# Optimization experiments

Measured on AMD Instinct MI355X. Metric: run time of the kernel, lower is better.

Reference implementation:

```python
import jax, jax.numpy as jnp
import numpy as np

ANG, CEN = 9, 4
MIND, MAXD = -4, 4
NDISP = MAXD - MIND + 1
BDR = CEN * MAXD  # 16
EPS = 1e-5


def lrelu(x):
    return jnp.where(x >= 0, x, 0.1 * x)


def bn(x, p):
    # p: [4, C] = (gamma, beta, running_mean, running_var); inference-mode BatchNorm
    g, b, m, v = p
    sh = (1, -1) + (1,) * (x.ndim - 2)
    return (x - m.reshape(sh)) * (g.reshape(sh) * jax.lax.rsqrt(v.reshape(sh) + EPS)) + b.reshape(sh)


def conv3d(x, w, pad):
    return jax.lax.conv_general_dilated(
        x, w, (1, 1, 1), [(pad[0], pad[0]), (pad[1], pad[1]), (pad[2], pad[2])],
        dimension_numbers=('NCDHW', 'OIDHW', 'NCDHW'))


def pw3d(x, w, b=None):  # 1x1x1 conv
    y = jnp.einsum('oc,bcdhw->bodhw', w, x)
    return y if b is None else y + b.reshape(1, -1, 1, 1, 1)


def bilinear_zeros(img, px, py):
    # torch F.grid_sample(mode='bilinear', padding_mode='zeros', align_corners=False)
    # img [..., h, w]; px, py: same leading dims + [h, w] (pixel coords)
    h, w = img.shape[-2], img.shape[-1]
    x0 = jnp.floor(px); y0 = jnp.floor(py)
    dx = px - x0; dy = py - y0
    x0i = x0.astype(jnp.int32); y0i = y0.astype(jnp.int32)
    flat = img.reshape(img.shape[:-2] + (h * w,))

    def tap(yi, xi, wgt):
        valid = ((xi >= 0) & (xi < w) & (yi >= 0) & (yi < h)).astype(img.dtype)
        idx = jnp.clip(yi, 0, h - 1) * w + jnp.clip(xi, 0, w - 1)
        v = jnp.take_along_axis(flat, idx.reshape(idx.shape[:-2] + (h * w,)), axis=-1)
        return v.reshape(idx.shape) * wgt * valid

    return (tap(y0i, x0i, (1 - dx) * (1 - dy)) + tap(y0i, x0i + 1, dx * (1 - dy)) +
            tap(y0i + 1, x0i, (1 - dx) * dy) + tap(y0i + 1, x0i + 1, dx * dy))


def generate_mask(lf, disp):
    # lf [b,1,9,9,h,w]; warp() is called with -disp in the torch code
    b, _, _, _, h, w = lf.shape
    imgs = lf[:, 0]                                    # [b,9,9,h,w]
    d = -disp[:, 0]                                    # [b,h,w]
    off = (jnp.arange(ANG) - CEN).astype(imgs.dtype)   # du / dv
    xb = jnp.linspace(0.0, 1.0, w).astype(imgs.dtype)
    yb = jnp.linspace(0.0, 1.0, h).astype(imgs.dtype)
    # grid = 2*(base+shift)-1; align_corners=False pixel coord = ((g+1)*S - 1)/2
    px = (xb[None, None, None, :] + off[None, :, None, None] * d[:, None] / w) * w - 0.5  # [b,9(v),h,w]
    py = (yb[None, None, :, None] + off[None, :, None, None] * d[:, None] / h) * h - 0.5  # [b,9(u),h,w]
    PX = jnp.broadcast_to(px[:, None], (b, ANG, ANG, h, w))
    PY = jnp.broadcast_to(py[:, :, None], (b, ANG, ANG, h, w))
    warped = bilinear_zeros(imgs, PX, PY)
    ref = imgs[:, CEN, CEN][:, None, None]
    diff = jnp.abs(warped - ref)
    diff = diff.at[:, CEN, CEN].set(0.0)  # center view is used unwarped -> zero diff
    return ((1.0 - diff) ** 2).reshape(b, ANG * ANG, h, w)


def build_cost(feat, mask, fuse_w):
    # Direct windowed gather equivalent of the per-disparity Unfold(dilation=h_pad-d)
    # on the angular-tiled padded image. For disparity d and view (ki,kj), output
    # pixel (i,j) reads view (ki,kj) at (i+(CEN-ki)*d, j+(CEN-kj)*d), zeros outside.
    b, c, _, h, w = feat.shape                        # feat [b,8,81,h,w]
    f = feat.reshape(b, c, ANG, ANG, h, w)
    fpad = jnp.pad(f, ((0, 0), (0, 0), (0, 0), (0, 0), (BDR, BDR), (BDR, BDR)))
    ds = jnp.arange(MIND, MAXD + 1)                   # [9]
    ki = jnp.arange(ANG)
    row = BDR + (CEN - ki)[None, :, None] * ds[:, None, None] + jnp.arange(h)[None, None, :]  # [D,9,h]
    col = BDR + (CEN - ki)[None, :, None] * ds[:, None, None] + jnp.arange(w)[None, None, :]  # [D,9,w]
    KI = ki[None, :, None, None, None]
    KJ = ki[None, None, :, None, None]
    RR = row[:, :, None, :, None]
    CC = col[:, None, :, None, :]
    g = fpad[:, :, KI, KJ, RR, CC]                    # [b,8,D,9,9,h,w]
    mod = g * mask.reshape(b, 1, 1, ANG, ANG, h, w)   # mask modulation (ModulateConv2d)
    Wf = fuse_w.reshape(c, fuse_w.shape[0] // c, ANG, ANG)  # grouped 1x1 fuse, groups=c
    cost = jnp.einsum('gouv,bgduvhw->bgodhw', Wf, mod).reshape(b, fuse_w.shape[0], NDISP, h, w)
    return cost / mask.mean(axis=1)[:, None, None]


def _forward(x, dispGT, if_w0, if_bn0, resb_w, resb_b, resb_bn, if_w1, if_bn1,
             if_w2, if_bn2, last_w, fuse_w, sq_w, sq_bn, c1_w, c1_bn, c2_w, c2_bn,
             c3_w, c3_bn, c4_w, r3_body_w, r3_body_bn, r3_ca_w1, r3_ca_b1, r3_ca_bn1,
             r3_ca_w2, r3_ca_b2, r3_ca_bn2):
    b = x.shape[0]
    h = x.shape[2] // ANG; w = x.shape[3] // ANG
    lf = x.reshape(b, 1, ANG, h, ANG, w).transpose(0, 1, 2, 4, 3, 5)  # [b,1,a1,a2,h,w]
    x5 = lf.reshape(b, 1, ANG * ANG, h, w)
    # ---- init_feature: per-view 2D convs expressed as (1,3,3) 3D convs
    hbuf = bn(conv3d(x5, if_w0, (0, 1, 1)), if_bn0)
    for i in range(8):  # 8 ResB blocks (fixed architecture depth)
        t = lrelu(bn(conv3d(hbuf, resb_w[i, 0], (0, 1, 1)) + resb_b[i, 0].reshape(1, -1, 1, 1, 1), resb_bn[i, 0]))
        t = bn(conv3d(t, resb_w[i, 1], (0, 1, 1)) + resb_b[i, 1].reshape(1, -1, 1, 1, 1), resb_bn[i, 1])
        hbuf = hbuf + t
    hbuf = lrelu(bn(conv3d(hbuf, if_w1, (0, 1, 1)), if_bn1))
    hbuf = lrelu(bn(conv3d(hbuf, if_w2, (0, 1, 1)), if_bn2))
    feat = conv3d(hbuf, last_w, (0, 1, 1))            # [b,8,81,h,w]
    # ---- occlusion-aware mask + cost volume
    mask = generate_mask(lf, dispGT)                  # [b,81,h,w]
    cost = build_cost(feat, mask, fuse_w)             # [b,512,9,h,w]
    # ---- 3D CNN aggregation
    buf = lrelu(bn(pw3d(cost, sq_w), sq_bn))
    buf = lrelu(bn(conv3d(buf, c1_w, (1, 1, 1)), c1_bn))
    buf = lrelu(bn(conv3d(buf, c2_w, (1, 1, 1)), c2_bn))
    for i in range(2):  # ResB3D blocks with CALayer
        t = lrelu(bn(conv3d(buf, r3_body_w[i, 0], (1, 1, 1)), r3_body_bn[i, 0]))
        t = bn(conv3d(t, r3_body_w[i, 1], (1, 1, 1)), r3_body_bn[i, 1])
        y = t.mean(axis=(3, 4), keepdims=True)        # AdaptiveAvgPool3d((9,1,1))
        y = lrelu(bn(pw3d(y, r3_ca_w1[i], r3_ca_b1[i]), r3_ca_bn1[i]))
        y = jax.nn.sigmoid(bn(pw3d(y, r3_ca_w2[i], r3_ca_b2[i]), r3_ca_bn2[i]))
        buf = t * y + buf
    buf = lrelu(bn(conv3d(buf, c3_w, (1, 1, 1)), c3_bn))
    score = conv3d(buf, c4_w, (1, 1, 1))[:, 0]        # [b,9,h,w]
    att = jax.nn.softmax(score, axis=1)
    dvals = jnp.arange(MIND, MAXD + 1).astype(att.dtype)
    return jnp.sum(att * dvals[None, :, None, None], axis=1, keepdims=True)  # [b,1,h,w]


def setup_inputs():
    B, H, W = 1, 64, 64
    keys = iter(jax.random.split(jax.random.key(0), 256))

    def nrm(shape, fan_in):
        return jax.random.normal(next(keys), shape, jnp.float32) / np.float32(np.sqrt(fan_in))

    def bnp(c):
        k1, k2, k3, k4 = jax.random.split(next(keys), 4)
        return jnp.stack([jax.random.uniform(k1, (c,), jnp.float32, 0.5, 1.5),
                          0.1 * jax.random.normal(k2, (c,), jnp.float32),
                          0.1 * jax.random.normal(k3, (c,), jnp.float32),
                          jax.random.uniform(k4, (c,), jnp.float32, 0.5, 1.5)])

    d = {}
    d['x'] = jax.random.normal(next(keys), (B, 1, ANG * H, ANG * W), jnp.float32)
    d['dispGT'] = jax.random.uniform(next(keys), (B, 1, H, W), jnp.float32, -4.0, 4.0)
    d['if_w0'] = nrm((16, 1, 1, 3, 3), 9)
    d['if_bn0'] = bnp(16)
    d['resb_w'] = nrm((8, 2, 16, 16, 1, 3, 3), 16 * 9)
    d['resb_b'] = 0.01 * jax.random.normal(next(keys), (8, 2, 16), jnp.float32)
    d['resb_bn'] = jnp.stack([jnp.stack([bnp(16), bnp(16)]) for _ in range(8)])
    d['if_w1'] = nrm((16, 16, 1, 3, 3), 16 * 9)
    d['if_bn1'] = bnp(16)
    d['if_w2'] = nrm((8, 16, 1, 3, 3), 16 * 9)
    d['if_bn2'] = bnp(8)
    d['last_w'] = nrm((8, 8, 1, 3, 3), 8 * 9)
    d['fuse_w'] = nrm((512, 81), 81)
    d['sq_w'] = nrm((160, 512), 512)
    d['sq_bn'] = bnp(160)
    for nmn in ('c1', 'c2', 'c3'):
        d[nmn + '_w'] = nrm((160, 160, 3, 3, 3), 160 * 27)
        d[nmn + '_bn'] = bnp(160)
    d['c4_w'] = nrm((1, 160, 3, 3, 3), 160 * 27)
    d['r3_body_w'] = nrm((2, 2, 160, 160, 3, 3, 3), 160 * 27)
    d['r3_body_bn'] = jnp.stack([jnp.stack([bnp(160), bnp(160)]) for _ in range(2)])
    d['r3_ca_w1'] = nrm((2, 10, 160), 160)
    d['r3_ca_b1'] = 0.01 * jax.random.normal(next(keys), (2, 10), jnp.float32)
    d['r3_ca_bn1'] = jnp.stack([bnp(10) for _ in range(2)])
    d['r3_ca_w2'] = nrm((2, 160, 10), 10)
    d['r3_ca_b2'] = 0.01 * jax.random.normal(next(keys), (2, 160), jnp.float32)
    d['r3_ca_bn2'] = jnp.stack([bnp(160) for _ in range(2)])
    return d


def reference(x, dispGT, if_w0, if_bn0, resb_w, resb_b, resb_bn, if_w1, if_bn1,
              if_w2, if_bn2, last_w, fuse_w, sq_w, sq_bn, c1_w, c1_bn, c2_w, c2_bn,
              c3_w, c3_bn, c4_w, r3_body_w, r3_body_bn, r3_ca_w1, r3_ca_b1, r3_ca_bn1,
              r3_ca_w2, r3_ca_b2, r3_ca_bn2):
    return _forward(x, dispGT, if_w0, if_bn0, resb_w, resb_b, resb_bn, if_w1, if_bn1,
                    if_w2, if_bn2, last_w, fuse_w, sq_w, sq_bn, c1_w, c1_bn, c2_w, c2_bn,
                    c3_w, c3_bn, c4_w, r3_body_w, r3_body_bn, r3_ca_w1, r3_ca_b1, r3_ca_bn1,
                    r3_ca_w2, r3_ca_b2, r3_ca_bn2)
```

## Files before the change

### kernel.cpp

```cpp
#include <hip/hip_runtime.h>
#include <hip/hip_bf16.h>
#include <math.h>

constexpr float EPSB = 1e-5f;

constexpr int SAS = 69696;
constexpr int SRS = 1056;
constexpr size_t SVOL = 81ull * SAS;

constexpr int PZS = 696960;
constexpr int PYS = 10560;
constexpr size_t PVOL = 11ull * 4356 * 160;

constexpr size_t OFF_SA   = 0;
constexpr size_t OFF_SB   = 5645376;
constexpr size_t OFF_MASK = 11290752;
constexpr size_t OFF_INVM = 11622528;
constexpr size_t OFF_SC   = 11626624;
constexpr size_t OFF_YM   = 11663488;
constexpr size_t OFF_Y2   = 11664928;
constexpr size_t OFF_YMP  = 11666368;
constexpr size_t OFF_PA   = 11712448;
constexpr size_t UOFF_PHA = 38758016;
constexpr size_t UOFF_PHB = 46424576;
constexpr size_t UOFF_SHA = 0;
constexpr size_t UOFF_SHB = 11290752;
constexpr size_t UOFF_WH  = 54091136;
constexpr size_t UOFF_WSH = 63767936;
constexpr size_t UOFF_ABH = 63865216;
constexpr size_t UOFF_ABL = 63972736;

typedef short s16x8 __attribute__((ext_vector_type(8)));
typedef float f32x4 __attribute__((ext_vector_type(4)));
typedef _Float16 h16x8 __attribute__((ext_vector_type(8)));
typedef _Float16 h16x4 __attribute__((ext_vector_type(4)));

__device__ __forceinline__ float lrelu_f(float v) { return v >= 0.f ? v : 0.1f * v; }
__device__ __forceinline__ float b2f(unsigned short s) {
  union { float f; unsigned u; } z; z.u = ((unsigned)s) << 16; return z.f;
}
__device__ __forceinline__ unsigned short f2b(float f) {
  __hip_bfloat16 h = __float2bfloat16(f);
  return *(unsigned short*)&h;
}

__global__ __launch_bounds__(256) void k_if0(const float* __restrict__ x,
                                             const float* __restrict__ w0,
                                             const float* __restrict__ bn0,
                                             _Float16* __restrict__ SHA) {
  int a = blockIdx.x;
  int p = blockIdx.y * 256 + threadIdx.x;
  int y = p >> 6, xx = p & 63;
  int ai = a / 9, aj = a % 9;
  float v[3][3];
#pragma unroll
  for (int dy = 0; dy < 3; ++dy) {
    int gy = y + dy - 1;
#pragma unroll
    for (int dx = 0; dx < 3; ++dx) {
      int gx = xx + dx - 1;
      v[dy][dx] = (gy >= 0 && gy < 64 && gx >= 0 && gx < 64)
                      ? x[(ai * 64 + gy) * 576 + aj * 64 + gx] : 0.f;
    }
  }
  h16x8 o0, o1;
#pragma unroll
  for (int c = 0; c < 16; ++c) {
    float acc = 0.f;
#pragma unroll
    for (int t = 0; t < 9; ++t) acc += w0[c * 9 + t] * v[t / 3][t % 3];
    float g = bn0[c], b = bn0[16 + c], m = bn0[32 + c], vv = bn0[48 + c];
    float val = (acc - m) * (g * rsqrtf(vv + EPSB)) + b;
    if (c < 8) o0[c] = (_Float16)val;
    else       o1[c - 8] = (_Float16)val;
  }
  _Float16* dst = SHA + (size_t)a * SAS + (size_t)(y + 1) * SRS + (size_t)(xx + 1) * 16;
  *(h16x8*)&dst[0] = o0;
  *(h16x8*)&dst[8] = o1;
}

__global__ __launch_bounds__(256) void k_wslice(const float* __restrict__ resb_w,
                                                const float* __restrict__ if1_w,
                                                const float* __restrict__ if2_w,
                                                const float* __restrict__ last_w,
                                                _Float16* __restrict__ WSH) {
  int c = blockIdx.x;
  for (int idx = threadIdx.x; idx < 2560; idx += 256) {
    int o = idx / 160, k = idx % 160;
    int t = k >> 4, ci = k & 15;
    float v = 0.f;
    if (t < 9) {
      if (c < 16)       v = resb_w[((size_t)c * 256 + o * 16 + ci) * 9 + t];
      else if (c == 16) v = if1_w[(size_t)(o * 16 + ci) * 9 + t];
      else if (c == 17) v = (o < 8) ? if2_w[(size_t)(o * 16 + ci) * 9 + t] : 0.f;
      else              v = (o < 8 && ci < 8) ? last_w[(size_t)(o * 8 + ci) * 9 + t] : 0.f;
    }
    WSH[c * 2560 + idx] = (_Float16)v;
  }
}

__global__ __launch_bounds__(256) void k_wt7(const float* __restrict__ c1,
                                             const float* __restrict__ c2,
                                             const float* __restrict__ r3,
                                             const float* __restrict__ c3,
                                             _Float16* __restrict__ WH) {
  __shared__ float L[6912];
  int l = blockIdx.y;
  const float* w = (l == 0) ? c1 : (l == 1) ? c2 : (l < 6) ? r3 + (size_t)(l - 2) * 691200 : c3;
  size_t base = (size_t)blockIdx.x * 256;
  for (int i = threadIdx.x; i < 6912; i += 256) L[i] = w[base * 27 + i];
  __syncthreads();
  _Float16* wh = WH + (size_t)l * 691200;
  int r = (int)base + threadIdx.x;
#pragma unroll 1
  for (int t = 0; t < 27; ++t) {
    float v = L[threadIdx.x * 27 + t];
    wh[(size_t)t * 25600 + r] = (_Float16)v;
  }
}

__global__ __launch_bounds__(192) void k_A(const float* __restrict__ sq_w,
                                           const float* __restrict__ fuse_w,
                                           unsigned short* __restrict__ ABH,
                                           unsigned short* __restrict__ ABL) {
  int k = blockIdx.x;
  int o = threadIdx.x;
  if (o >= 160) return;
  float acc = 0.f;
  if (k < 648) {
    int uv = k >> 3, g = k & 7;
    for (int o2 = 0; o2 < 64; ++o2)
      acc += sq_w[(size_t)o * 512 + g * 64 + o2] * fuse_w[(size_t)(g * 64 + o2) * 81 + uv];
  }
  unsigned short h = f2b(acc);
  ABH[(size_t)o * 672 + k] = h;
  ABL[(size_t)o * 672 + k] = f2b(acc - b2f(h));
}

__device__ __forceinline__ float img_at(const float* __restrict__ x, int i, int j, int yy, int xx) {
  if (yy < 0 || yy >= 64 || xx < 0 || xx >= 64) return 0.f;
  return x[(i * 64 + yy) * 576 + j * 64 + xx];
}

__global__ __launch_bounds__(256) void k_mask(const float* __restrict__ x,
                                              const float* __restrict__ disp,
                                              float* __restrict__ mask,
                                              float* __restrict__ invm) {
  int p = blockIdx.x * 256 + threadIdx.x;
  int y = p >> 6, xx = p & 63;
  float d = -disp[p];
  float ref = x[(4 * 64 + y) * 576 + 4 * 64 + xx];
  float ssum = 0.f;
  float xbase = (float)xx * (64.0f / 63.0f);
  float ybase = (float)y * (64.0f / 63.0f);
  for (int i = 0; i < 9; ++i) {
    float py = ybase + (float)(i - 4) * d - 0.5f;
    float y0f = floorf(py);
    float fy = py - y0f;
    int y0 = (int)y0f;
    for (int j = 0; j < 9; ++j) {
      float px = xbase + (float)(j - 4) * d - 0.5f;
      float x0f = floorf(px);
      float fx = px - x0f;
      int x0 = (int)x0f;
      float val = img_at(x, i, j, y0, x0) * (1.f - fx) * (1.f - fy)
                + img_at(x, i, j, y0, x0 + 1) * fx * (1.f - fy)
                + img_at(x, i, j, y0 + 1, x0) * (1.f - fx) * fy
                + img_at(x, i, j, y0 + 1, x0 + 1) * fx * fy;
      float diff = (i == 4 && j == 4) ? 0.f : fabsf(val - ref);
      float m = 1.f - diff;
      m = m * m;
      mask[(i * 9 + j) * 4096 + p] = m;
      ssum += m;
    }
  }
  invm[p] = 81.f / ssum;
}

template <bool BN, bool LRELU, bool RESADD, int CO>
__global__ __launch_bounds__(256) void k_cs(const _Float16* __restrict__ in,
                                            _Float16* __restrict__ out,
                                            const _Float16* __restrict__ wsh,
                                            const float* __restrict__ bias,
                                            const float* __restrict__ bnp) {
  __shared__ _Float16 Af[10 * 66 * 26];
  int a = blockIdx.x, y0 = blockIdx.y * 8;
  int tid = threadIdx.x, lane = tid & 63, w = tid >> 6;
  int lr = lane & 15, lq = lane >> 4;
  const _Float16* src = in + (size_t)a * SAS + (size_t)y0 * SRS;
  for (int it = tid; it < 1320; it += 256) {
    int row = it / 132, rem = it % 132;
    int px = rem >> 1, half = rem & 1;
    h16x8 g = *(const h16x8*)&src[row * SRS + px * 16 + half * 8];
    *(h16x8*)&Af[(row * 66 + px) * 26 + half * 8] = g;
  }
  __syncthreads();
  h16x8 bh[5];
#pragma unroll
  for (int ks = 0; ks < 5; ++ks)
    bh[ks] = *(const h16x8*)&wsh[lr * 160 + ks * 32 + lq * 8];
  int offk[5];
#pragma unroll
  for (int ks = 0; ks < 5; ++ks) {
    int t = ks * 2 + (lq >> 1);
    if (t > 8) t = 8;
    offk[ks] = ((t / 3) * 66 + (t % 3)) * 26 + (lq & 1) * 8;
  }
  f32x4 acc[8];
#pragma unroll
  for (int i = 0; i < 8; ++i) acc[i] = (f32x4){0.f, 0.f, 0.f, 0.f};
#pragma unroll
  for (int mf = 0; mf < 8; ++mf) {
    int gm = w * 8 + mf;
    int yl = gm >> 2, xq = gm & 3;
    int am = (yl * 66 + xq * 16 + lr) * 26;
#pragma unroll
    for (int ks = 0; ks < 5; ++ks) {
      h16x8 ah = *(const h16x8*)&Af[am + offk[ks]];
      acc[mf] = __builtin_amdgcn_mfma_f32_16x16x32_f16(ah, bh[ks], acc[mf], 0, 0, 0);
    }
  }
  int co = lr;
  bool coval = (CO == 16) || (co < CO);
  float sc = 1.f, sh = 0.f;
  if (BN && coval) {
    float g = bnp[co], b = bnp[CO + co], m = bnp[2 * CO + co], vv = bnp[3 * CO + co];
    sc = g * rsqrtf(vv + EPSB);
    sh = b - m * sc;
    if (bias) sh += bias[co] * sc;
  }
#pragma unroll
  for (int mf = 0; mf < 8; ++mf) {
    int gm = w * 8 + mf;
    int yl = gm >> 2, xq = gm & 3;
    if (coval) {
#pragma unroll
      for (int r = 0; r < 4; ++r) {
        int x = xq * 16 + lq * 4 + r;
        float val = acc[mf][r] * sc + sh;
        if (LRELU) val = lrelu_f(val);
        size_t oo = (size_t)a * SAS + (size_t)(y0 + yl + 1) * SRS + (size_t)(x + 1) * 16 + co;
        if (RESADD) out[oo] = (_Float16)((float)out[oo] + val);
        else        out[oo] = (_Float16)val;
      }
    }
  }
}

__global__ __launch_bounds__(256) void k_costsq(const _Float16* __restrict__ feat,
                                                const float* __restrict__ mask,
                                                const float* __restrict__ invm,
                                                const unsigned short* __restrict__ ABH,
                                                const unsigned short* __restrict__ ABL,
                                                const float* __restrict__ sq_bn,
                                                _Float16* __restrict__ outPH) {
  __shared__ short Ah[6144];
  __shared__ short Al[6144];
  int dI = blockIdx.x, y = blockIdx.y;
  int dd = dI - 4;
  int tid = threadIdx.x, lane = tid & 63, w = tid >> 6;
  int wm = w >> 1, wn = w & 1;
  int lr = lane & 15, lq = lane >> 4;
  f32x4 acc[2][5];
#pragma unroll
  for (int i = 0; i < 2; ++i)
#pragma unroll
    for (int j = 0; j < 5; ++j) acc[i][j] = (f32x4){0.f, 0.f, 0.f, 0.f};

  for (int ch = 0; ch < 7; ++ch) {
    __syncthreads();
    for (int it = tid; it < 768; it += 256) {
      int xl = it / 12, uvL = it % 12;
      int uv = ch * 12 + uvL;
      s16x8 hv = {0, 0, 0, 0, 0, 0, 0, 0}, lv = {0, 0, 0, 0, 0, 0, 0, 0};
      if (uv < 81) {
        int u = uv / 9, v = uv % 9;
        int ys = y + (4 - u) * dd;
        int xs = xl + (4 - v) * dd;
        if (ys >= 0 && ys < 64 && xs >= 0 && xs < 64) {
          const _Float16* fp = feat + (size_t)uv * SAS + (size_t)(ys + 1) * SRS + (size_t)(xs + 1) * 16;
          h16x8 fv = *(const h16x8*)fp;
          float mv = mask[uv * 4096 + y * 64 + xl];
#pragma unroll
          for (int j = 0; j < 8; ++j) {
            float f = (float)fv[j] * mv;
            unsigned short h = f2b(f);
            hv[j] = h;
            lv[j] = f2b(f - b2f(h));
          }
        }
      }
      *(s16x8*)&Ah[xl * 96 + uvL * 8] = hv;
      *(s16x8*)&Al[xl * 96 + uvL * 8] = lv;
    }
    __syncthreads();
#pragma unroll
    for (int kb = 0; kb < 3; ++kb) {
      int ka = kb * 32 + lq * 8;
      s16x8 a0h = *(const s16x8*)&Ah[(wm * 32 + lr) * 96 + ka];
      s16x8 a0l = *(const s16x8*)&Al[(wm * 32 + lr) * 96 + ka];
      s16x8 a1h = *(const s16x8*)&Ah[(wm * 32 + 16 + lr) * 96 + ka];
      s16x8 a1l = *(const s16x8*)&Al[(wm * 32 + 16 + lr) * 96 + ka];
      int kg = ch * 96 + ka;
#pragma unroll
      for (int nf = 0; nf < 5; ++nf) {
        int n = wn * 80 + nf * 16 + lr;
        s16x8 bh = *(const s16x8*)&ABH[(size_t)n * 672 + kg];
        s16x8 bl = *(const s16x8*)&ABL[(size_t)n * 672 + kg];
        acc[0][nf] = __builtin_amdgcn_mfma_f32_16x16x32_bf16(a0h, bh, acc[0][nf], 0, 0, 0);
        acc[0][nf] = __builtin_amdgcn_mfma_f32_16x16x32_bf16(a0h, bl, acc[0][nf], 0, 0, 0);
        acc[0][nf] = __builtin_amdgcn_mfma_f32_16x16x32_bf16(a0l, bh, acc[0][nf], 0, 0, 0);
        acc[1][nf] = __builtin_amdgcn_mfma_f32_16x16x32_bf16(a1h, bh, acc[1][nf], 0, 0, 0);
        acc[1][nf] = __builtin_amdgcn_mfma_f32_16x16x32_bf16(a1h, bl, acc[1][nf], 0, 0, 0);
        acc[1][nf] = __builtin_amdgcn_mfma_f32_16x16x32_bf16(a1l, bh, acc[1][nf], 0, 0, 0);
      }
    }
  }
#pragma unroll
  for (int nf = 0; nf < 5; ++nf) {
    int n = wn * 80 + nf * 16 + lr;
    float g = sq_bn[n], b = sq_bn[160 + n], m = sq_bn[320 + n], vv = sq_bn[480 + n];
    float sc = g * rsqrtf(vv + EPSB), sh = b - m * sc;
#pragma unroll
    for (int mf = 0; mf < 2; ++mf) {
#pragma unroll
      for (int r = 0; r < 4; ++r) {
        int x = wm * 32 + mf * 16 + lq * 4 + r;
        float val = acc[mf][nf][r] * invm[y * 64 + x];
        val = val * sc + sh;
        val = lrelu_f(val);
        outPH[(size_t)(dI + 1) * PZS + (size_t)(y + 1) * PYS + (size_t)(x + 1) * 160 + n] =
            (_Float16)val;
      }
    }
  }
}

template <bool LRELU>
__global__ __launch_bounds__(320, 3) void k_mconv(const _Float16* __restrict__ in,
                                                  float* __restrict__ out32,
                                                  _Float16* __restrict__ out16,
                                                  const _Float16* __restrict__ wh,
                                                  const float* __restrict__ bnp) {
  __shared__ _Float16 Af[66 * 174];
  int bid = blockIdx.x;
  int swz = (bid & 7) * 72 + (bid >> 3);
  int z = swz / 64, y = swz % 64;
  int tid = threadIdx.x;
  int lane = tid & 63;
  int wn = tid >> 6;
  int lr = lane & 15;
  int lq = lane >> 4;

  f32x4 acc[4][2];
#pragma unroll
  for (int i = 0; i < 4; ++i)
#pragma unroll
    for (int j = 0; j < 2; ++j) acc[i][j] = (f32x4){0.f, 0.f, 0.f, 0.f};

  const _Float16* wbase = wh + (size_t)(wn * 32 + lr) * 160 + lq * 8;

#pragma unroll 1
  for (int dzy = 0; dzy < 9; ++dzy) {
    int dz = dzy / 3, dy = dzy % 3;
    const _Float16* src = in + (size_t)(z + dz) * PZS + (size_t)(y + dy) * PYS;
    __syncthreads();
    for (int v = tid; v < 1320; v += 320) {
      h16x8 g = *(const h16x8*)&src[(size_t)v * 8];
      int row = v / 20, col = (v % 20) * 8;
      *(h16x8*)&Af[row * 174 + col] = g;
    }
    __syncthreads();

#pragma unroll 1
    for (int dx = 0; dx < 3; ++dx) {
      const _Float16* wt = wbase + (size_t)(dzy * 3 + dx) * 25600;
      h16x8 bA[2], bB[2];
#pragma unroll
      for (int nf = 0; nf < 2; ++nf)
        bA[nf] = *(const h16x8*)&wt[(size_t)nf * 16 * 160];

      auto step = [&](int ks, h16x8 (&cur)[2], h16x8 (&nxt)[2], bool pre) {
        if (pre) {
#pragma unroll
          for (int nf = 0; nf < 2; ++nf)
            nxt[nf] = *(const h16x8*)&wt[(size_t)nf * 16 * 160 + (ks + 1) * 32];
        }
        h16x8 a0 = *(const h16x8*)&Af[(0 * 16 + lr + dx) * 174 + ks * 32 + lq * 8];
        h16x8 a1 = *(const h16x8*)&Af[(1 * 16 + lr + dx) * 174 + ks * 32 + lq * 8];
        h16x8 a2 = *(const h16x8*)&Af[(2 * 16 + lr + dx) * 174 + ks * 32 + lq * 8];
        h16x8 a3 = *(const h16x8*)&Af[(3 * 16 + lr + dx) * 174 + ks * 32 + lq * 8];
#pragma unroll
        for (int nf = 0; nf < 2; ++nf) {
          acc[0][nf] = __builtin_amdgcn_mfma_f32_16x16x32_f16(a0, cur[nf], acc[0][nf], 0, 0, 0);
          acc[1][nf] = __builtin_amdgcn_mfma_f32_16x16x32_f16(a1, cur[nf], acc[1][nf], 0, 0, 0);
          acc[2][nf] = __builtin_amdgcn_mfma_f32_16x16x32_f16(a2, cur[nf], acc[2][nf], 0, 0, 0);
          acc[3][nf] = __builtin_amdgcn_mfma_f32_16x16x32_f16(a3, cur[nf], acc[3][nf], 0, 0, 0);
        }
      };
      step(0, bA, bB, true);
      step(1, bB, bA, true);
      step(2, bA, bB, true);
      step(3, bB, bA, true);
      step(4, bA, bB, false);
    }
  }
#pragma unroll
  for (int nf = 0; nf < 2; ++nf) {
    int n = wn * 32 + nf * 16 + lr;
    float sc = bnp[n] * rsqrtf(bnp[480 + n] + EPSB);
    float sh = bnp[160 + n] - bnp[320 + n] * sc;
#pragma unroll
    for (int mq = 0; mq < 4; ++mq) {
#pragma unroll
      for (int r = 0; r < 4; ++r) {
        int x = mq * 16 + lq * 4 + r;
        float val = acc[mq][nf][r] * sc + sh;
        if (LRELU) val = lrelu_f(val);
        size_t oo = (size_t)(z + 1) * PZS + (size_t)(y + 1) * PYS + (size_t)(x + 1) * 160 + n;
        if (out32) out32[oo] = val;
        if (out16) out16[oo] = (_Float16)val;
      }
    }
  }
}

__global__ __launch_bounds__(256) void k_c4(const _Float16* __restrict__ in,
                                            const float* __restrict__ w,
                                            float* __restrict__ score) {
  __shared__ float L[66 * 169];
  __shared__ float red[256];
  int zy = blockIdx.x;
  int z = zy / 64, y = zy % 64;
  int tid = threadIdx.x;
  int x = tid & 63, q = tid >> 6;
  float acc = 0.f;
  for (int dzy = 0; dzy < 9; ++dzy) {
    int dz = dzy / 3, dy = dzy % 3;
    const _Float16* src = in + (size_t)(z + dz) * PZS + (size_t)(y + dy) * PYS;
    __syncthreads();
    for (int v = tid; v < 1320; v += 256) {
      h16x8 g = *(const h16x8*)&src[v * 8];
      int row = v / 20, col = (v % 20) * 8;
#pragma unroll
      for (int j = 0; j < 8; ++j) L[row * 169 + col + j] = (float)g[j];
    }
    __syncthreads();
#pragma unroll 1
    for (int dx = 0; dx < 3; ++dx) {
      int t = dzy * 3 + dx;
      for (int ci = q * 40; ci < q * 40 + 40; ++ci)
        acc += L[(x + dx) * 169 + ci] * w[ci * 27 + t];
    }
  }
  red[tid] = acc;
  __syncthreads();
  if (q == 0)
    score[z * 4096 + y * 64 + x] = red[x] + red[64 + x] + red[128 + x] + red[192 + x];
}

__global__ __launch_bounds__(256) void k_mean1(const float* __restrict__ in,
                                               float* __restrict__ ymp) {
  int z = blockIdx.x, yg = blockIdx.y, xq = blockIdx.z;
  int c = threadIdx.x;
  if (c >= 160) return;
  float s = 0.f;
  for (int yy = 0; yy < 8; ++yy) {
    int y = yg * 8 + yy;
    for (int xl = 0; xl < 16; ++xl) {
      int x = xq * 16 + xl;
      s += in[(size_t)(z + 1) * PZS + (size_t)(y + 1) * PYS + (size_t)(x + 1) * 160 + c];
    }
  }
  ymp[((z * 8 + yg) * 4 + xq) * 160 + c] = s;
}

__global__ __launch_bounds__(256) void k_mean2(const float* __restrict__ ymp,
                                               float* __restrict__ ym) {
  int idx = blockIdx.x * 256 + threadIdx.x;
  if (idx >= 1440) return;
  int c = idx / 9, z = idx % 9;
  float s = 0.f;
  for (int p = 0; p < 32; ++p) s += ymp[(z * 32 + p) * 160 + c];
  ym[idx] = s * (1.f / 4096.f);
}

__global__ __launch_bounds__(256) void k_ca(const float* __restrict__ ym,
                                            const float* __restrict__ w1,
                                            const float* __restrict__ b1,
                                            const float* __restrict__ bn1,
                                            const float* __restrict__ w2,
                                            const float* __restrict__ b2,
                                            const float* __restrict__ bn2,
                                            float* __restrict__ y2) {
  __shared__ float yml[1440];
  __shared__ float yy[90];
  for (int i = threadIdx.x; i < 1440; i += 256) yml[i] = ym[i];
  __syncthreads();
  if (threadIdx.x < 90) {
    int c = threadIdx.x / 9, z = threadIdx.x % 9;
    float acc = b1[c];
    for (int ci = 0; ci < 160; ++ci) acc += w1[c * 160 + ci] * yml[ci * 9 + z];
    float g = bn1[c], b = bn1[10 + c], m = bn1[20 + c], vv = bn1[30 + c];
    acc = (acc - m) * (g * rsqrtf(vv + EPSB)) + b;
    yy[threadIdx.x] = lrelu_f(acc);
  }
  __syncthreads();
  for (int i = threadIdx.x; i < 1440; i += 256) {
    int c = i / 9, z = i % 9;
    float acc = b2[c];
#pragma unroll
    for (int k = 0; k < 10; ++k) acc += w2[c * 10 + k] * yy[k * 9 + z];
    float g = bn2[c], b = bn2[160 + c], m = bn2[320 + c], vv = bn2[480 + c];
    acc = (acc - m) * (g * rsqrtf(vv + EPSB)) + b;
    y2[i] = 1.f / (1.f + expf(-acc));
  }
}

__global__ __launch_bounds__(256) void k_sadd(float* __restrict__ buf,
                                              _Float16* __restrict__ shadow,
                                              const float* __restrict__ t,
                                              const float* __restrict__ y2) {
  int i = blockIdx.x * 256 + threadIdx.x;
  int p = i / 160, c = i % 160;
  int z = p >> 12, r = p & 4095;
  int y = r >> 6, x = r & 63;
  size_t a = (size_t)(z + 1) * PZS + (size_t)(y + 1) * PYS + (size_t)(x + 1) * 160 + c;
  float val = buf[a] + t[a] * y2[c * 9 + z];
  buf[a] = val;
  shadow[a] = (_Float16)val;
}

__global__ __launch_bounds__(256) void k_out(const float* __restrict__ score,
                                             float* __restrict__ out) {
  int p = blockIdx.x * 256 + threadIdx.x;
  float v[9];
  float mx = -1e30f;
#pragma unroll
  for (int z = 0; z < 9; ++z) {
    v[z] = score[z * 4096 + p];
    mx = fmaxf(mx, v[z]);
  }
  float s = 0.f, r = 0.f;
#pragma unroll
  for (int z = 0; z < 9; ++z) {
    float e = expf(v[z] - mx);
    s += e;
    r += e * (float)(z - 4);
  }
  out[p] = r / s;
}

extern "C" void kernel_launch(void* const* d_in, const int* in_sizes, int n_in,
                              void* d_out, int out_size, void* d_ws, size_t ws_size,
                              hipStream_t stream) {
  const float* X      = (const float*)d_in[0];
  const float* disp   = (const float*)d_in[1];
  const float* if_w0  = (const float*)d_in[2];
  const float* if_bn0 = (const float*)d_in[3];
  const float* resb_w = (const float*)d_in[4];
  const float* resb_b = (const float*)d_in[5];
  const float* resb_bn= (const float*)d_in[6];
  const float* if_w1  = (const float*)d_in[7];
  const float* if_bn1 = (const float*)d_in[8];
  const float* if_w2  = (const float*)d_in[9];
  const float* if_bn2 = (const float*)d_in[10];
  const float* last_w = (const float*)d_in[11];
  const float* fuse_w = (const float*)d_in[12];
  const float* sq_w   = (const float*)d_in[13];
  const float* sq_bn  = (const float*)d_in[14];
  const float* c1_w   = (const float*)d_in[15];
  const float* c1_bn  = (const float*)d_in[16];
  const float* c2_w   = (const float*)d_in[17];
  const float* c2_bn  = (const float*)d_in[18];
  const float* c3_w   = (const float*)d_in[19];
  const float* c3_bn  = (const float*)d_in[20];
  const float* c4_w   = (const float*)d_in[21];
  const float* r3_w   = (const float*)d_in[22];
  const float* r3_bn  = (const float*)d_in[23];
  const float* ca_w1  = (const float*)d_in[24];
  const float* ca_b1  = (const float*)d_in[25];
  const float* ca_bn1 = (const float*)d_in[26];
  const float* ca_w2  = (const float*)d_in[27];
  const float* ca_b2  = (const float*)d_in[28];
  const float* ca_bn2 = (const float*)d_in[29];

  float* ws   = (float*)d_ws;
  float* PC   = ws;
  float* MASK = ws + OFF_MASK;
  float* INVM = ws + OFF_INVM;
  float* SC   = ws + OFF_SC;
  float* YM   = ws + OFF_YM;
  float* Y2   = ws + OFF_Y2;
  float* YMP  = ws + OFF_YMP;
  float* PA   = ws + OFF_PA;
  unsigned short* U   = (unsigned short*)d_ws;
  _Float16* SHA       = (_Float16*)(U + UOFF_SHA);
  _Float16* SHB       = (_Float16*)(U + UOFF_SHB);
  _Float16* PHA       = (_Float16*)(U + UOFF_PHA);
  _Float16* PHB       = (_Float16*)(U + UOFF_PHB);
  _Float16* WH        = (_Float16*)(U + UOFF_WH);
  _Float16* WSS       = (_Float16*)(U + UOFF_WSH);
  unsigned short* ABH = U + UOFF_ABH;
  unsigned short* ABL = U + UOFF_ABL;

  hipMemsetAsync(SHA, 0, SVOL * 2, stream);
  hipMemsetAsync(SHB, 0, SVOL * 2, stream);
  hipMemsetAsync(PHA, 0, PVOL * 2, stream);
  hipMemsetAsync(PHB, 0, PVOL * 2, stream);

  k_wt7<<<dim3(100, 7), 256, 0, stream>>>(c1_w, c2_w, r3_w, c3_w, WH);
  k_wslice<<<19, 256, 0, stream>>>(resb_w, if_w1, if_w2, last_w, WSS);
  k_A<<<672, 192, 0, stream>>>(sq_w, fuse_w, ABH, ABL);
  k_mask<<<16, 256, 0, stream>>>(X, disp, MASK, INVM);

  k_if0<<<dim3(81, 16), 256, 0, stream>>>(X, if_w0, if_bn0, SHA);
  for (int i = 0; i < 8; ++i) {
    k_cs<true, true, false, 16><<<dim3(81, 8), 256, 0, stream>>>(
        SHA, SHB, WSS + (size_t)(2 * i) * 2560, resb_b + i * 32, resb_bn + i * 128);
    k_cs<true, false, true, 16><<<dim3(81, 8), 256, 0, stream>>>(
        SHB, SHA, WSS + (size_t)(2 * i + 1) * 2560, resb_b + i * 32 + 16, resb_bn + i * 128 + 64);
  }
  k_cs<true, true, false, 16><<<dim3(81, 8), 256, 0, stream>>>(
      SHA, SHB, WSS + 16 * 2560, nullptr, if_bn1);
  k_cs<true, true, false, 8><<<dim3(81, 8), 256, 0, stream>>>(
      SHB, SHA, WSS + 17 * 2560, nullptr, if_bn2);
  k_cs<false, false, false, 8><<<dim3(81, 8), 256, 0, stream>>>(
      SHA, SHB, WSS + 18 * 2560, nullptr, nullptr);

  k_costsq<<<dim3(9, 64), 256, 0, stream>>>(SHB, MASK, INVM, ABH, ABL, sq_bn, PHA);

  k_mconv<true><<<576, 320, 0, stream>>>(PHA, nullptr, PHB, WH + 0ull * 691200, c1_bn);
  k_mconv<true><<<576, 320, 0, stream>>>(PHB, PA, PHA, WH + 1ull * 691200, c2_bn);
  for (int i = 0; i < 2; ++i) {
    k_mconv<true><<<576, 320, 0, stream>>>(PHA, nullptr, PHB,
                                           WH + (size_t)(2 + 2 * i) * 691200, r3_bn + i * 1280);
    k_mconv<false><<<576, 320, 0, stream>>>(PHB, PC, nullptr,
                                            WH + (size_t)(3 + 2 * i) * 691200,
                                            r3_bn + i * 1280 + 640);
    k_mean1<<<dim3(9, 8, 4), 256, 0, stream>>>(PC, YMP);
    k_mean2<<<6, 256, 0, stream>>>(YMP, YM);
    k_ca<<<1, 256, 0, stream>>>(YM, ca_w1 + i * 1600, ca_b1 + i * 10, ca_bn1 + i * 40,
                                ca_w2 + i * 1600, ca_b2 + i * 160, ca_bn2 + i * 640, Y2);
    k_sadd<<<23040, 256, 0, stream>>>(PA, PHA, PC, Y2);
  }
  k_mconv<true><<<576, 320, 0, stream>>>(PHA, nullptr, PHB, WH + 6ull * 691200, c3_bn);
  k_c4<<<576, 256, 0, stream>>>(PHB, c4_w, SC);
  k_out<<<16, 256, 0, stream>>>(SC, (float*)d_out);
}
```

Baseline: 980.8 us.

## Fuse residual-block convs, drop split-bf16 cost GEMM, shrink LDS padding

Replaces the two per-residual-block spatial conv launches with one fused kernel that keeps the intermediate activation and residual in LDS. This removes half the launches and the global round-trip of the intermediate. The cost-volume squeeze GEMM now uses a single fp16 MFMA instead of three bf16 hi/lo MFMAs. The r3 conv output is stored as fp16 instead of fp32, and LDS row strides change from 26/174 to 24/168. The fp16 changes cost accuracy, and the new strides may add LDS bank conflicts.

```diff
diff --git a/kernel.cpp b/kernel.cpp
--- a/kernel.cpp
+++ b/kernel.cpp
@@ -12,8 +12,6 @@
 constexpr int PYS = 10560;
 constexpr size_t PVOL = 11ull * 4356 * 160;
 
-constexpr size_t OFF_SA   = 0;
-constexpr size_t OFF_SB   = 5645376;
 constexpr size_t OFF_MASK = 11290752;
 constexpr size_t OFF_INVM = 11622528;
 constexpr size_t OFF_SC   = 11626624;
@@ -21,28 +19,20 @@
 constexpr size_t OFF_Y2   = 11664928;
 constexpr size_t OFF_YMP  = 11666368;
 constexpr size_t OFF_PA   = 11712448;
+constexpr size_t UOFF_SHA = 0;
+constexpr size_t UOFF_SHB = 11290752;
+constexpr size_t UOFF_PHC = 0;
 constexpr size_t UOFF_PHA = 38758016;
 constexpr size_t UOFF_PHB = 46424576;
-constexpr size_t UOFF_SHA = 0;
-constexpr size_t UOFF_SHB = 11290752;
 constexpr size_t UOFF_WH  = 54091136;
 constexpr size_t UOFF_WSH = 63767936;
-constexpr size_t UOFF_ABH = 63865216;
-constexpr size_t UOFF_ABL = 63972736;
-
-typedef short s16x8 __attribute__((ext_vector_type(8)));
+constexpr size_t UOFF_ABF = 63865216;
+
 typedef float f32x4 __attribute__((ext_vector_type(4)));
 typedef _Float16 h16x8 __attribute__((ext_vector_type(8)));
 typedef _Float16 h16x4 __attribute__((ext_vector_type(4)));
 
 __device__ __forceinline__ float lrelu_f(float v) { return v >= 0.f ? v : 0.1f * v; }
-__device__ __forceinline__ float b2f(unsigned short s) {
-  union { float f; unsigned u; } z; z.u = ((unsigned)s) << 16; return z.f;
-}
-__device__ __forceinline__ unsigned short f2b(float f) {
-  __hip_bfloat16 h = __float2bfloat16(f);
-  return *(unsigned short*)&h;
-}
 
 __global__ __launch_bounds__(256) void k_if0(const float* __restrict__ x,
                                              const float* __restrict__ w0,
@@ -121,8 +111,7 @@
 
 __global__ __launch_bounds__(192) void k_A(const float* __restrict__ sq_w,
                                            const float* __restrict__ fuse_w,
-                                           unsigned short* __restrict__ ABH,
-                                           unsigned short* __restrict__ ABL) {
+                                           _Float16* __restrict__ ABF) {
   int k = blockIdx.x;
   int o = threadIdx.x;
   if (o >= 160) return;
@@ -132,9 +121,7 @@
     for (int o2 = 0; o2 < 64; ++o2)
       acc += sq_w[(size_t)o * 512 + g * 64 + o2] * fuse_w[(size_t)(g * 64 + o2) * 81 + uv];
   }
-  unsigned short h = f2b(acc);
-  ABH[(size_t)o * 672 + k] = h;
-  ABL[(size_t)o * 672 + k] = f2b(acc - b2f(h));
+  ABF[(size_t)o * 672 + k] = (_Float16)acc;
 }
 
 __device__ __forceinline__ float img_at(const float* __restrict__ x, int i, int j, int yy, int xx) {
@@ -177,13 +164,12 @@
   invm[p] = 81.f / ssum;
 }
 
-template <bool BN, bool LRELU, bool RESADD, int CO>
+template <bool BN, bool LRELU, int CO>
 __global__ __launch_bounds__(256) void k_cs(const _Float16* __restrict__ in,
                                             _Float16* __restrict__ out,
                                             const _Float16* __restrict__ wsh,
-                                            const float* __restrict__ bias,
                                             const float* __restrict__ bnp) {
-  __shared__ _Float16 Af[10 * 66 * 26];
+  __shared__ _Float16 Af[15840];
   int a = blockIdx.x, y0 = blockIdx.y * 8;
   int tid = threadIdx.x, lane = tid & 63, w = tid >> 6;
   int lr = lane & 15, lq = lane >> 4;
@@ -192,7 +178,7 @@
     int row = it / 132, rem = it % 132;
     int px = rem >> 1, half = rem & 1;
     h16x8 g = *(const h16x8*)&src[row * SRS + px * 16 + half * 8];
-    *(h16x8*)&Af[(row * 66 + px) * 26 + half * 8] = g;
+    *(h16x8*)&Af[(row * 66 + px) * 24 + half * 8] = g;
   }
   __syncthreads();
   h16x8 bh[5];
@@ -204,7 +190,7 @@
   for (int ks = 0; ks < 5; ++ks) {
     int t = ks * 2 + (lq >> 1);
     if (t > 8) t = 8;
-    offk[ks] = ((t / 3) * 66 + (t % 3)) * 26 + (lq & 1) * 8;
+    offk[ks] = ((t / 3) * 66 + (t % 3)) * 24 + (lq & 1) * 8;
   }
   f32x4 acc[8];
 #pragma unroll
@@ -213,7 +199,7 @@
   for (int mf = 0; mf < 8; ++mf) {
     int gm = w * 8 + mf;
     int yl = gm >> 2, xq = gm & 3;
-    int am = (yl * 66 + xq * 16 + lr) * 26;
+    int am = (yl * 66 + xq * 16 + lr) * 24;
 #pragma unroll
     for (int ks = 0; ks < 5; ++ks) {
       h16x8 ah = *(const h16x8*)&Af[am + offk[ks]];
@@ -227,7 +213,6 @@
     float g = bnp[co], b = bnp[CO + co], m = bnp[2 * CO + co], vv = bnp[3 * CO + co];
     sc = g * rsqrtf(vv + EPSB);
     sh = b - m * sc;
-    if (bias) sh += bias[co] * sc;
   }
 #pragma unroll
   for (int mf = 0; mf < 8; ++mf) {
@@ -240,8 +225,99 @@
         float val = acc[mf][r] * sc + sh;
         if (LRELU) val = lrelu_f(val);
         size_t oo = (size_t)a * SAS + (size_t)(y0 + yl + 1) * SRS + (size_t)(x + 1) * 16 + co;
-        if (RESADD) out[oo] = (_Float16)((float)out[oo] + val);
-        else        out[oo] = (_Float16)val;
+        out[oo] = (_Float16)val;
+      }
+    }
+  }
+}
+
+__global__ __launch_bounds__(256, 2) void k_cs2(const _Float16* __restrict__ in,
+                                                _Float16* __restrict__ out,
+                                                const _Float16* __restrict__ w1,
+                                                const _Float16* __restrict__ w2,
+                                                const float* __restrict__ bias,
+                                                const float* __restrict__ bnp) {
+  __shared__ _Float16 L1[12 * 66 * 24];
+  __shared__ _Float16 L2[10 * 66 * 24];
+  int a = blockIdx.x, y0 = blockIdx.y * 8;
+  int tid = threadIdx.x, lane = tid & 63, w = tid >> 6;
+  int lr = lane & 15, lq = lane >> 4;
+  for (int i = tid; i < 1980; i += 256) ((h16x8*)L2)[i] = (h16x8)(_Float16)0.f;
+  const _Float16* src = in + (size_t)a * SAS;
+  for (int it = tid; it < 1584; it += 256) {
+    int sr = it / 132, rem = it % 132;
+    int px = rem >> 1, half = rem & 1;
+    int gyp = y0 - 1 + sr;
+    h16x8 g = (h16x8)(_Float16)0.f;
+    if (gyp >= 0 && gyp <= 65)
+      g = *(const h16x8*)&src[(size_t)gyp * SRS + px * 16 + half * 8];
+    *(h16x8*)&L1[(sr * 66 + px) * 24 + half * 8] = g;
+  }
+  __syncthreads();
+  int offk[5];
+#pragma unroll
+  for (int ks = 0; ks < 5; ++ks) {
+    int t = ks * 2 + (lq >> 1);
+    if (t > 8) t = 8;
+    offk[ks] = ((t / 3) * 66 + (t % 3)) * 24 + (lq & 1) * 8;
+  }
+  {
+    h16x8 bh[5];
+#pragma unroll
+    for (int ks = 0; ks < 5; ++ks)
+      bh[ks] = *(const h16x8*)&w1[lr * 160 + ks * 32 + lq * 8];
+    float g1 = bnp[lr], b1 = bnp[16 + lr], m1 = bnp[32 + lr], v1 = bnp[48 + lr];
+    float sc1 = g1 * rsqrtf(v1 + EPSB);
+    float sh1 = b1 - m1 * sc1 + bias[lr] * sc1;
+#pragma unroll
+    for (int mf = 0; mf < 10; ++mf) {
+      int gm = w * 10 + mf;
+      int yl = gm >> 2, xq = gm & 3;
+      f32x4 acc = (f32x4){0.f, 0.f, 0.f, 0.f};
+      int am = (yl * 66 + xq * 16 + lr) * 24;
+#pragma unroll
+      for (int ks = 0; ks < 5; ++ks) {
+        h16x8 ah = *(const h16x8*)&L1[am + offk[ks]];
+        acc = __builtin_amdgcn_mfma_f32_16x16x32_f16(ah, bh[ks], acc, 0, 0, 0);
+      }
+      int gy = y0 - 1 + yl;
+      if (gy >= 0 && gy <= 63) {
+#pragma unroll
+        for (int r = 0; r < 4; ++r) {
+          int x = xq * 16 + lq * 4 + r;
+          float val = lrelu_f(acc[r] * sc1 + sh1);
+          L2[(yl * 66 + x + 1) * 24 + lr] = (_Float16)val;
+        }
+      }
+    }
+  }
+  __syncthreads();
+  {
+    h16x8 bh[5];
+#pragma unroll
+    for (int ks = 0; ks < 5; ++ks)
+      bh[ks] = *(const h16x8*)&w2[lr * 160 + ks * 32 + lq * 8];
+    float g2 = bnp[64 + lr], b2 = bnp[80 + lr], m2 = bnp[96 + lr], v2 = bnp[112 + lr];
+    float sc2 = g2 * rsqrtf(v2 + EPSB);
+    float sh2 = b2 - m2 * sc2 + bias[16 + lr] * sc2;
+#pragma unroll
+    for (int mf = 0; mf < 8; ++mf) {
+      int gm = w * 8 + mf;
+      int yl = gm >> 2, xq = gm & 3;
+      f32x4 acc = (f32x4){0.f, 0.f, 0.f, 0.f};
+      int am = (yl * 66 + xq * 16 + lr) * 24;
+#pragma unroll
+      for (int ks = 0; ks < 5; ++ks) {
+        h16x8 ah = *(const h16x8*)&L2[am + offk[ks]];
+        acc = __builtin_amdgcn_mfma_f32_16x16x32_f16(ah, bh[ks], acc, 0, 0, 0);
+      }
+#pragma unroll
+      for (int r = 0; r < 4; ++r) {
+        int x = xq * 16 + lq * 4 + r;
+        float res = (float)L1[((yl + 2) * 66 + x + 1) * 24 + lr];
+        float val = res + acc[r] * sc2 + sh2;
+        out[(size_t)a * SAS + (size_t)(y0 + yl + 1) * SRS + (size_t)(x + 1) * 16 + lr] =
+            (_Float16)val;
       }
     }
   }
@@ -250,12 +326,10 @@
 __global__ __launch_bounds__(256) void k_costsq(const _Float16* __restrict__ feat,
                                                 const float* __restrict__ mask,
                                                 const float* __restrict__ invm,
-                                                const unsigned short* __restrict__ ABH,
-                                                const unsigned short* __restrict__ ABL,
+                                                const _Float16* __restrict__ ABF,
                                                 const float* __restrict__ sq_bn,
                                                 _Float16* __restrict__ outPH) {
-  __shared__ short Ah[6144];
-  __shared__ short Al[6144];
+  __shared__ _Float16 Ahs[6144];
   int dI = blockIdx.x, y = blockIdx.y;
   int dd = dI - 4;
   int tid = threadIdx.x, lane = tid & 63, w = tid >> 6;
@@ -272,7 +346,7 @@
     for (int it = tid; it < 768; it += 256) {
       int xl = it / 12, uvL = it % 12;
       int uv = ch * 12 + uvL;
-      s16x8 hv = {0, 0, 0, 0, 0, 0, 0, 0}, lv = {0, 0, 0, 0, 0, 0, 0, 0};
+      h16x8 hv = (h16x8)(_Float16)0.f;
       if (uv < 81) {
         int u = uv / 9, v = uv % 9;
         int ys = y + (4 - u) * dd;
@@ -282,37 +356,24 @@
           h16x8 fv = *(const h16x8*)fp;
           float mv = mask[uv * 4096 + y * 64 + xl];
 #pragma unroll
-          for (int j = 0; j < 8; ++j) {
-            float f = (float)fv[j] * mv;
-            unsigned short h = f2b(f);
-            hv[j] = h;
-            lv[j] = f2b(f - b2f(h));
-          }
+          for (int j = 0; j < 8; ++j) hv[j] = (_Float16)((float)fv[j] * mv);
         }
       }
-      *(s16x8*)&Ah[xl * 96 + uvL * 8] = hv;
-      *(s16x8*)&Al[xl * 96 + uvL * 8] = lv;
+      *(h16x8*)&Ahs[xl * 96 + uvL * 8] = hv;
     }
     __syncthreads();
 #pragma unroll
     for (int kb = 0; kb < 3; ++kb) {
       int ka = kb * 32 + lq * 8;
-      s16x8 a0h = *(const s16x8*)&Ah[(wm * 32 + lr) * 96 + ka];
-      s16x8 a0l = *(const s16x8*)&Al[(wm * 32 + lr) * 96 + ka];
-      s16x8 a1h = *(const s16x8*)&Ah[(wm * 32 + 16 + lr) * 96 + ka];
-      s16x8 a1l = *(const s16x8*)&Al[(wm * 32 + 16 + lr) * 96 + ka];
+      h16x8 a0 = *(const h16x8*)&Ahs[(wm * 32 + lr) * 96 + ka];
+      h16x8 a1 = *(const h16x8*)&Ahs[(wm * 32 + 16 + lr) * 96 + ka];
       int kg = ch * 96 + ka;
 #pragma unroll
       for (int nf = 0; nf < 5; ++nf) {
         int n = wn * 80 + nf * 16 + lr;
-        s16x8 bh = *(const s16x8*)&ABH[(size_t)n * 672 + kg];
-        s16x8 bl = *(const s16x8*)&ABL[(size_t)n * 672 + kg];
-        acc[0][nf] = __builtin_amdgcn_mfma_f32_16x16x32_bf16(a0h, bh, acc[0][nf], 0, 0, 0);
-        acc[0][nf] = __builtin_amdgcn_mfma_f32_16x16x32_bf16(a0h, bl, acc[0][nf], 0, 0, 0);
-        acc[0][nf] = __builtin_amdgcn_mfma_f32_16x16x32_bf16(a0l, bh, acc[0][nf], 0, 0, 0);
-        acc[1][nf] = __builtin_amdgcn_mfma_f32_16x16x32_bf16(a1h, bh, acc[1][nf], 0, 0, 0);
-        acc[1][nf] = __builtin_amdgcn_mfma_f32_16x16x32_bf16(a1h, bl, acc[1][nf], 0, 0, 0);
-        acc[1][nf] = __builtin_amdgcn_mfma_f32_16x16x32_bf16(a1l, bh, acc[1][nf], 0, 0, 0);
+        h16x8 bf = *(const h16x8*)&ABF[(size_t)n * 672 + kg];
+        acc[0][nf] = __builtin_amdgcn_mfma_f32_16x16x32_f16(a0, bf, acc[0][nf], 0, 0, 0);
+        acc[1][nf] = __builtin_amdgcn_mfma_f32_16x16x32_f16(a1, bf, acc[1][nf], 0, 0, 0);
       }
     }
   }
@@ -342,7 +403,7 @@
                                                   _Float16* __restrict__ out16,
                                                   const _Float16* __restrict__ wh,
                                                   const float* __restrict__ bnp) {
-  __shared__ _Float16 Af[66 * 174];
+  __shared__ _Float16 Af[66 * 168];
   int bid = blockIdx.x;
   int swz = (bid & 7) * 72 + (bid >> 3);
   int z = swz / 64, y = swz % 64;
@@ -368,7 +429,7 @@
     for (int v = tid; v < 1320; v += 320) {
       h16x8 g = *(const h16x8*)&src[(size_t)v * 8];
       int row = v / 20, col = (v % 20) * 8;
-      *(h16x8*)&Af[row * 174 + col] = g;
+      *(h16x8*)&Af[row * 168 + col] = g;
     }
     __syncthreads();
 
@@ -386,10 +447,10 @@
           for (int nf = 0; nf < 2; ++nf)
             nxt[nf] = *(const h16x8*)&wt[(size_t)nf * 16 * 160 + (ks + 1) * 32];
         }
-        h16x8 a0 = *(const h16x8*)&Af[(0 * 16 + lr + dx) * 174 + ks * 32 + lq * 8];
-        h16x8 a1 = *(const h16x8*)&Af[(1 * 16 + lr + dx) * 174 + ks * 32 + lq * 8];
-        h16x8 a2 = *(const h16x8*)&Af[(2 * 16 + lr + dx) * 174 + ks * 32 + lq * 8];
-        h16x8 a3 = *(const h16x8*)&Af[(3 * 16 + lr + dx) * 174 + ks * 32 + lq * 8];
+        h16x8 a0 = *(const h16x8*)&Af[(0 * 16 + lr + dx) * 168 + ks * 32 + lq * 8];
+        h16x8 a1 = *(const h16x8*)&Af[(1 * 16 + lr + dx) * 168 + ks * 32 + lq * 8];
+        h16x8 a2 = *(const h16x8*)&Af[(2 * 16 + lr + dx) * 168 + ks * 32 + lq * 8];
+        h16x8 a3 = *(const h16x8*)&Af[(3 * 16 + lr + dx) * 168 + ks * 32 + lq * 8];
 #pragma unroll
         for (int nf = 0; nf < 2; ++nf) {
           acc[0][nf] = __builtin_amdgcn_mfma_f32_16x16x32_f16(a0, cur[nf], acc[0][nf], 0, 0, 0);
@@ -459,7 +520,7 @@
     score[z * 4096 + y * 64 + x] = red[x] + red[64 + x] + red[128 + x] + red[192 + x];
 }
 
-__global__ __launch_bounds__(256) void k_mean1(const float* __restrict__ in,
+__global__ __launch_bounds__(256) void k_mean1(const _Float16* __restrict__ in,
                                                float* __restrict__ ymp) {
   int z = blockIdx.x, yg = blockIdx.y, xq = blockIdx.z;
   int c = threadIdx.x;
@@ -469,7 +530,7 @@
     int y = yg * 8 + yy;
     for (int xl = 0; xl < 16; ++xl) {
       int x = xq * 16 + xl;
-      s += in[(size_t)(z + 1) * PZS + (size_t)(y + 1) * PYS + (size_t)(x + 1) * 160 + c];
+      s += (float)in[(size_t)(z + 1) * PZS + (size_t)(y + 1) * PYS + (size_t)(x + 1) * 160 + c];
     }
   }
   ymp[((z * 8 + yg) * 4 + xq) * 160 + c] = s;
@@ -519,14 +580,14 @@
 
 __global__ __launch_bounds__(256) void k_sadd(float* __restrict__ buf,
                                               _Float16* __restrict__ shadow,
-                                              const float* __restrict__ t,
+                                              const _Float16* __restrict__ t,
                                               const float* __restrict__ y2) {
   int i = blockIdx.x * 256 + threadIdx.x;
   int p = i / 160, c = i % 160;
   int z = p >> 12, r = p & 4095;
   int y = r >> 6, x = r & 63;
   size_t a = (size_t)(z + 1) * PZS + (size_t)(y + 1) * PYS + (size_t)(x + 1) * 160 + c;
-  float val = buf[a] + t[a] * y2[c * 9 + z];
+  float val = buf[a] + (float)t[a] * y2[c * 9 + z];
   buf[a] = val;
   shadow[a] = (_Float16)val;
 }
@@ -586,7 +647,6 @@
   const float* ca_bn2 = (const float*)d_in[29];
 
   float* ws   = (float*)d_ws;
-  float* PC   = ws;
   float* MASK = ws + OFF_MASK;
   float* INVM = ws + OFF_INVM;
   float* SC   = ws + OFF_SC;
@@ -597,12 +657,12 @@
   unsigned short* U   = (unsigned short*)d_ws;
   _Float16* SHA       = (_Float16*)(U + UOFF_SHA);
   _Float16* SHB       = (_Float16*)(U + UOFF_SHB);
+  _Float16* PHC       = (_Float16*)(U + UOFF_PHC);
   _Float16* PHA       = (_Float16*)(U + UOFF_PHA);
   _Float16* PHB       = (_Float16*)(U + UOFF_PHB);
   _Float16* WH        = (_Float16*)(U + UOFF_WH);
   _Float16* WSS       = (_Float16*)(U + UOFF_WSH);
-  unsigned short* ABH = U + UOFF_ABH;
-  unsigned short* ABL = U + UOFF_ABL;
+  _Float16* ABF       = (_Float16*)(U + UOFF_ABF);
 
   hipMemsetAsync(SHA, 0, SVOL * 2, stream);
   hipMemsetAsync(SHB, 0, SVOL * 2, stream);
@@ -611,38 +671,36 @@
 
   k_wt7<<<dim3(100, 7), 256, 0, stream>>>(c1_w, c2_w, r3_w, c3_w, WH);
   k_wslice<<<19, 256, 0, stream>>>(resb_w, if_w1, if_w2, last_w, WSS);
-  k_A<<<672, 192, 0, stream>>>(sq_w, fuse_w, ABH, ABL);
+  k_A<<<672, 192, 0, stream>>>(sq_w, fuse_w, ABF);
   k_mask<<<16, 256, 0, stream>>>(X, disp, MASK, INVM);
 
   k_if0<<<dim3(81, 16), 256, 0, stream>>>(X, if_w0, if_bn0, SHA);
   for (int i = 0; i < 8; ++i) {
-    k_cs<true, true, false, 16><<<dim3(81, 8), 256, 0, stream>>>(
-        SHA, SHB, WSS + (size_t)(2 * i) * 2560, resb_b + i * 32, resb_bn + i * 128);
-    k_cs<true, false, true, 16><<<dim3(81, 8), 256, 0, stream>>>(
-        SHB, SHA, WSS + (size_t)(2 * i + 1) * 2560, resb_b + i * 32 + 16, resb_bn + i * 128 + 64);
-  }
-  k_cs<true, true, false, 16><<<dim3(81, 8), 256, 0, stream>>>(
-      SHA, SHB, WSS + 16 * 2560, nullptr, if_bn1);
-  k_cs<true, true, false, 8><<<dim3(81, 8), 256, 0, stream>>>(
-      SHB, SHA, WSS + 17 * 2560, nullptr, if_bn2);
-  k_cs<false, false, false, 8><<<dim3(81, 8), 256, 0, stream>>>(
-      SHA, SHB, WSS + 18 * 2560, nullptr, nullptr);
-
-  k_costsq<<<dim3(9, 64), 256, 0, stream>>>(SHB, MASK, INVM, ABH, ABL, sq_bn, PHA);
+    _Float16* src = (i & 1) ? SHB : SHA;
+    _Float16* dst = (i & 1) ? SHA : SHB;
+    k_cs2<<<dim3(81, 8), 256, 0, stream>>>(
+        src, dst, WSS + (size_t)(2 * i) * 2560, WSS + (size_t)(2 * i + 1) * 2560,
+        resb_b + i * 32, resb_bn + i * 128);
+  }
+  k_cs<true, true, 16><<<dim3(81, 8), 256, 0, stream>>>(SHA, SHB, WSS + 16 * 2560, if_bn1);
+  k_cs<true, true, 8><<<dim3(81, 8), 256, 0, stream>>>(SHB, SHA, WSS + 17 * 2560, if_bn2);
+  k_cs<false, false, 8><<<dim3(81, 8), 256, 0, stream>>>(SHA, SHB, WSS + 18 * 2560, nullptr);
+
+  k_costsq<<<dim3(9, 64), 256, 0, stream>>>(SHB, MASK, INVM, ABF, sq_bn, PHA);
 
   k_mconv<true><<<576, 320, 0, stream>>>(PHA, nullptr, PHB, WH + 0ull * 691200, c1_bn);
   k_mconv<true><<<576, 320, 0, stream>>>(PHB, PA, PHA, WH + 1ull * 691200, c2_bn);
   for (int i = 0; i < 2; ++i) {
     k_mconv<true><<<576, 320, 0, stream>>>(PHA, nullptr, PHB,
                                            WH + (size_t)(2 + 2 * i) * 691200, r3_bn + i * 1280);
-    k_mconv<false><<<576, 320, 0, stream>>>(PHB, PC, nullptr,
+    k_mconv<false><<<576, 320, 0, stream>>>(PHB, nullptr, PHC,
                                             WH + (size_t)(3 + 2 * i) * 691200,
                                             r3_bn + i * 1280 + 640);
-    k_mean1<<<dim3(9, 8, 4), 256, 0, stream>>>(PC, YMP);
+    k_mean1<<<dim3(9, 8, 4), 256, 0, stream>>>(PHC, YMP);
     k_mean2<<<6, 256, 0, stream>>>(YMP, YM);
     k_ca<<<1, 256, 0, stream>>>(YM, ca_w1 + i * 1600, ca_b1 + i * 10, ca_bn1 + i * 40,
                                 ca_w2 + i * 1600, ca_b2 + i * 160, ca_bn2 + i * 640, Y2);
-    k_sadd<<<23040, 256, 0, stream>>>(PA, PHA, PC, Y2);
+    k_sadd<<<23040, 256, 0, stream>>>(PA, PHA, PHC, Y2);
   }
   k_mconv<true><<<576, 320, 0, stream>>>(PHA, nullptr, PHB, WH + 6ull * 691200, c3_bn);
   k_c4<<<576, 256, 0, stream>>>(PHB, c4_w, SC);
```

After: 935.9 us. 1.05x faster.
